# Kernel optimization log

Hardware: AMD Instinct MI355X
Metric: run time of the kernel (lower is better)

Reference implementation:

```python
import jax, jax.numpy as jnp
import numpy as np

B, C, N, K = 4, 64, 8192, 16
OUT = 128

def setup_inputs() -> dict:
    key = jax.random.key(0)
    k1, k2, k3, k4 = jax.random.split(key, 4)
    x = jax.random.normal(k1, (B, C, N, 1), dtype=jnp.float32)
    edge_index = jax.random.randint(k2, (2, B, N, K), 0, N)
    # BasicConv([2C, OUT]) is a 1x1 Conv2d -> weight [OUT, 2C], bias [OUT]
    W_nn = jax.random.normal(k3, (OUT, 2 * C), dtype=jnp.float32) * 0.02
    b_nn = jax.random.normal(k4, (OUT,), dtype=jnp.float32) * 0.02
    return {"x": x, "edge_index": edge_index, "W_nn": W_nn, "b_nn": b_nn}

def _gather_nodes(x2, idx):
    # x2: [B, C, N], idx: [B, N, K] -> [B, C, N, K]
    return jax.vmap(lambda xb, ib: xb[:, ib])(x2, idx)

def reference(x, edge_index, W_nn, b_nn):
    b, c, n, _ = x.shape
    x2 = x[:, :, :, 0]                      # [B, C, N]
    x_i = _gather_nodes(x2, edge_index[1])  # [B, C, N, K]
    x_j = _gather_nodes(x2, edge_index[0])  # [B, C, N, K]
    x_j = jnp.max(x_j - x_i, axis=-1, keepdims=True)  # [B, C, N, 1]
    # interleave channels: cat([x.unsqueeze(2), x_j.unsqueeze(2)], dim=2).reshape(b, 2c, n, 1)
    h = jnp.concatenate([x[:, :, None], x_j[:, :, None]], axis=2).reshape(b, 2 * c, n, 1)
    # BasicConv: 1x1 conv + bias + ReLU
    out = jnp.einsum('oc,bcn->bon', W_nn, h[:, :, :, 0]) + b_nn[None, :, None]
    return jax.nn.relu(out)[:, :, :, None]  # [B, OUT, N, 1]
```

## Files before the change

### kernel.cpp

```cpp
#include <hip/hip_runtime.h>
#include <cstddef>

#define BB 4
#define CC 64
#define NN 8192
#define KK 16
#define OO 128

#define SW 136
#define SH 136

typedef __attribute__((ext_vector_type(8))) short bf16x8;
typedef __attribute__((ext_vector_type(4))) float f32x4;

__device__ __forceinline__ unsigned short f2b(float f) {
    unsigned u = __builtin_bit_cast(unsigned, f);
    unsigned r = (u + 0x7fffu + ((u >> 16) & 1u)) >> 16;
    return (unsigned short)r;
}

__device__ __forceinline__ float bclo(unsigned d) {
    return __builtin_bit_cast(float, d << 16);
}
__device__ __forceinline__ float bchi(unsigned d) {
    return __builtin_bit_cast(float, d & 0xffff0000u);
}

__global__ __launch_bounds__(256) void transpose_kernel(
        const float* __restrict__ x, unsigned short* __restrict__ xt,
        const float* __restrict__ W, unsigned short* __restrict__ Wbf) {
    __shared__ float tile[64][65];
    const int b  = blockIdx.y;
    const int n0 = blockIdx.x * 64;
    const int t  = threadIdx.x;
    const int ln = t & 63;
    const int r  = t >> 6;

    const float* xb = x + (size_t)b * CC * NN;
    #pragma unroll
    for (int s = 0; s < 64; s += 4) {
        int c = s + r;
        tile[c][ln] = xb[(size_t)c * NN + n0 + ln];
    }
    __syncthreads();
    unsigned short* xtb = xt + ((size_t)b * NN + n0) * CC;
    #pragma unroll
    for (int s = 0; s < 64; s += 4) {
        int n = s + r;
        xtb[n * CC + ln] = f2b(tile[ln][n]);
    }

    if (b == 0 && blockIdx.x < 16) {
        int idx = blockIdx.x * 1024 + t * 4;
        float4 v = *reinterpret_cast<const float4*>(W + idx);
        ushort4 o;
        o.x = f2b(v.x); o.y = f2b(v.y); o.z = f2b(v.z); o.w = f2b(v.w);
        *reinterpret_cast<ushort4*>(Wbf + idx) = o;
    }
}

__global__ __launch_bounds__(256) void main_kernel(
        const unsigned short* __restrict__ xt,
        const unsigned short* __restrict__ Wbf,
        const int*            __restrict__ eidx,
        const float*          __restrict__ bias,
        float*                __restrict__ out) {
    __shared__ unsigned short Wl[128 * SW];
    __shared__ unsigned short hl[64 * SH];
    __shared__ int eL[2048];

    const int t    = threadIdx.x;
    const int lane = t & 63;
    const int w    = t >> 6;
    const int b    = blockIdx.y;
    const int n_base = blockIdx.x * 64;

    const int* e0 = eidx + ((size_t)b * NN + n_base) * KK;
    const int* e1 = e0 + (size_t)BB * NN * KK;
    *reinterpret_cast<int4*>(&eL[t * 4])        = *reinterpret_cast<const int4*>(e0 + t * 4);
    *reinterpret_cast<int4*>(&eL[1024 + t * 4]) = *reinterpret_cast<const int4*>(e1 + t * 4);

    #pragma unroll
    for (int it = 0; it < 8; it++) {
        int flat = it * 2048 + t * 8;
        int row = flat >> 7, col = flat & 127;
        *reinterpret_cast<int4*>(&Wl[row * SW + col]) =
            *reinterpret_cast<const int4*>(Wbf + flat);
    }
    __syncthreads();

    const unsigned short* xtb = xt + (size_t)b * NN * CC;
    const int g = lane >> 3;
    const int p = lane & 7;

    #pragma unroll
    for (int bt = 0; bt < 2; bt++) {
        const int nl = w * 16 + bt * 8 + g;
        uint4 xr = *reinterpret_cast<const uint4*>(xtb + (size_t)(n_base + nl) * CC + p * 8);

        float m[8];
        #pragma unroll
        for (int j = 0; j < 8; j++) m[j] = -1e30f;

        #pragma unroll
        for (int k = 0; k < KK; k++) {
            int ij = eL[nl * KK + k];
            int ii = eL[1024 + nl * KK + k];
            uint4 xj = *reinterpret_cast<const uint4*>(xtb + (size_t)ij * CC + p * 8);
            uint4 xi = *reinterpret_cast<const uint4*>(xtb + (size_t)ii * CC + p * 8);
            m[0] = fmaxf(m[0], bclo(xj.x) - bclo(xi.x));
            m[1] = fmaxf(m[1], bchi(xj.x) - bchi(xi.x));
            m[2] = fmaxf(m[2], bclo(xj.y) - bclo(xi.y));
            m[3] = fmaxf(m[3], bchi(xj.y) - bchi(xi.y));
            m[4] = fmaxf(m[4], bclo(xj.z) - bclo(xi.z));
            m[5] = fmaxf(m[5], bchi(xj.z) - bchi(xi.z));
            m[6] = fmaxf(m[6], bclo(xj.w) - bclo(xi.w));
            m[7] = fmaxf(m[7], bchi(xj.w) - bchi(xi.w));
        }

        unsigned xs[8];
        xs[0] = xr.x & 0xffffu; xs[1] = xr.x >> 16;
        xs[2] = xr.y & 0xffffu; xs[3] = xr.y >> 16;
        xs[4] = xr.z & 0xffffu; xs[5] = xr.z >> 16;
        xs[6] = xr.w & 0xffffu; xs[7] = xr.w >> 16;
        unsigned od[8];
        #pragma unroll
        for (int j = 0; j < 8; j++)
            od[j] = xs[j] | ((unsigned)f2b(m[j]) << 16);

        unsigned short* dst = &hl[nl * SH + p * 16];
        uint4 lo, hi;
        lo.x = od[0]; lo.y = od[1]; lo.z = od[2]; lo.w = od[3];
        hi.x = od[4]; hi.y = od[5]; hi.z = od[6]; hi.w = od[7];
        *reinterpret_cast<uint4*>(dst)     = lo;
        *reinterpret_cast<uint4*>(dst + 8) = hi;
    }
    __syncthreads();

    const int quad = lane >> 4;
    const int l15  = lane & 15;
    const int o0w  = w * 32;

    bf16x8 afr[2][4];
    #pragma unroll
    for (int ot = 0; ot < 2; ot++)
        #pragma unroll
        for (int ks = 0; ks < 4; ks++) {
            const unsigned short* ap = &Wl[(o0w + ot * 16 + l15) * SW + ks * 32 + quad * 8];
            afr[ot][ks] = *reinterpret_cast<const bf16x8*>(ap);
        }

    #pragma unroll
    for (int nt = 0; nt < 4; nt++) {
        f32x4 acc0 = {0.f, 0.f, 0.f, 0.f};
        f32x4 acc1 = {0.f, 0.f, 0.f, 0.f};
        #pragma unroll
        for (int ks = 0; ks < 4; ks++) {
            const unsigned short* bp = &hl[(nt * 16 + l15) * SH + ks * 32 + quad * 8];
            bf16x8 bfr = *reinterpret_cast<const bf16x8*>(bp);
            acc0 = __builtin_amdgcn_mfma_f32_16x16x32_bf16(afr[0][ks], bfr, acc0, 0, 0, 0);
            acc1 = __builtin_amdgcn_mfma_f32_16x16x32_bf16(afr[1][ks], bfr, acc1, 0, 0, 0);
        }
        int n_g = n_base + nt * 16 + l15;
        #pragma unroll
        for (int r = 0; r < 4; r++) {
            int o_a = o0w + quad * 4 + r;
            int o_b = o0w + 16 + quad * 4 + r;
            float va = acc0[r] + bias[o_a];
            float vb = acc1[r] + bias[o_b];
            out[((size_t)b * OO + o_a) * NN + n_g] = fmaxf(va, 0.f);
            out[((size_t)b * OO + o_b) * NN + n_g] = fmaxf(vb, 0.f);
        }
    }
}

extern "C" void kernel_launch(void* const* d_in, const int* in_sizes, int n_in,
                              void* d_out, int out_size, void* d_ws, size_t ws_size,
                              hipStream_t stream) {
    const float* x    = (const float*)d_in[0];
    const int*   eidx = (const int*)d_in[1];
    const float* W    = (const float*)d_in[2];
    const float* bias = (const float*)d_in[3];
    float* out = (float*)d_out;

    unsigned short* xt  = (unsigned short*)d_ws;
    unsigned short* Wbf = (unsigned short*)((char*)d_ws + 4 * 1024 * 1024);

    dim3 blk(256);
    dim3 grid(NN / 64, BB);
    transpose_kernel<<<grid, blk, 0, stream>>>(x, xt, W, Wbf);
    main_kernel<<<grid, blk, 0, stream>>>(xt, Wbf, eidx, bias, out);
}
```

Measured before the change: 82.46 us.

## Use 512-thread blocks, drop shared W staging, load MFMA A-fragments from global

The main kernel now runs 512 threads per block, so each thread handles one node's gather-max instead of two and each wave computes 16 output channels instead of 32. The 34 KB shared-memory copy of the weight matrix is removed; each wave loads its A-fragments and bias vector directly from global memory (L2-resident) before the barrier. The aim is to cut shared-memory use and the W staging work, allowing more resident waves to hide gather latency. In exchange, the redundant global W reads and smaller per-wave MFMA tiles add some overhead.

```diff
diff --git a/kernel.cpp b/kernel.cpp
--- a/kernel.cpp
+++ b/kernel.cpp
@@ -7,7 +7,6 @@
 #define KK 16
 #define OO 128
 
-#define SW 136
 #define SH 136
 
 typedef __attribute__((ext_vector_type(8))) short bf16x8;
@@ -59,13 +58,12 @@
     }
 }
 
-__global__ __launch_bounds__(256) void main_kernel(
+__global__ __launch_bounds__(512, 4) void main_kernel(
         const unsigned short* __restrict__ xt,
         const unsigned short* __restrict__ Wbf,
         const int*            __restrict__ eidx,
         const float*          __restrict__ bias,
         float*                __restrict__ out) {
-    __shared__ unsigned short Wl[128 * SW];
     __shared__ unsigned short hl[64 * SH];
     __shared__ int eL[2048];
 
@@ -75,59 +73,66 @@
     const int b    = blockIdx.y;
     const int n_base = blockIdx.x * 64;
 
+    const int quad = lane >> 4;
+    const int l15  = lane & 15;
+    const int o0   = w * 16;
+
+    bf16x8 afr[4];
+    #pragma unroll
+    for (int ks = 0; ks < 4; ks++)
+        afr[ks] = *reinterpret_cast<const bf16x8*>(
+            Wbf + (o0 + l15) * 128 + ks * 32 + quad * 8);
+    f32x4 bv = *reinterpret_cast<const f32x4*>(bias + o0 + quad * 4);
+
     const int* e0 = eidx + ((size_t)b * NN + n_base) * KK;
     const int* e1 = e0 + (size_t)BB * NN * KK;
-    *reinterpret_cast<int4*>(&eL[t * 4])        = *reinterpret_cast<const int4*>(e0 + t * 4);
-    *reinterpret_cast<int4*>(&eL[1024 + t * 4]) = *reinterpret_cast<const int4*>(e1 + t * 4);
+    if (t < 256) {
+        *reinterpret_cast<int4*>(&eL[t * 4]) =
+            *reinterpret_cast<const int4*>(e0 + t * 4);
+    } else {
+        int u = t - 256;
+        *reinterpret_cast<int4*>(&eL[1024 + u * 4]) =
+            *reinterpret_cast<const int4*>(e1 + u * 4);
+    }
+
+    const unsigned short* xtb = xt + (size_t)b * NN * CC;
+    const int nl = t >> 3;
+    const int p  = t & 7;
+    uint4 xr = *reinterpret_cast<const uint4*>(xtb + (size_t)(n_base + nl) * CC + p * 8);
+
+    __syncthreads();
+
+    float m[8];
+    #pragma unroll
+    for (int j = 0; j < 8; j++) m[j] = -1e30f;
 
     #pragma unroll
-    for (int it = 0; it < 8; it++) {
-        int flat = it * 2048 + t * 8;
-        int row = flat >> 7, col = flat & 127;
-        *reinterpret_cast<int4*>(&Wl[row * SW + col]) =
-            *reinterpret_cast<const int4*>(Wbf + flat);
+    for (int k = 0; k < KK; k++) {
+        int ij = eL[nl * KK + k];
+        int ii = eL[1024 + nl * KK + k];
+        uint4 xj = *reinterpret_cast<const uint4*>(xtb + (size_t)ij * CC + p * 8);
+        uint4 xi = *reinterpret_cast<const uint4*>(xtb + (size_t)ii * CC + p * 8);
+        m[0] = fmaxf(m[0], bclo(xj.x) - bclo(xi.x));
+        m[1] = fmaxf(m[1], bchi(xj.x) - bchi(xi.x));
+        m[2] = fmaxf(m[2], bclo(xj.y) - bclo(xi.y));
+        m[3] = fmaxf(m[3], bchi(xj.y) - bchi(xi.y));
+        m[4] = fmaxf(m[4], bclo(xj.z) - bclo(xi.z));
+        m[5] = fmaxf(m[5], bchi(xj.z) - bchi(xi.z));
+        m[6] = fmaxf(m[6], bclo(xj.w) - bclo(xi.w));
+        m[7] = fmaxf(m[7], bchi(xj.w) - bchi(xi.w));
     }
-    __syncthreads();
 
-    const unsigned short* xtb = xt + (size_t)b * NN * CC;
-    const int g = lane >> 3;
-    const int p = lane & 7;
+    unsigned xs[8];
+    xs[0] = xr.x & 0xffffu; xs[1] = xr.x >> 16;
+    xs[2] = xr.y & 0xffffu; xs[3] = xr.y >> 16;
+    xs[4] = xr.z & 0xffffu; xs[5] = xr.z >> 16;
+    xs[6] = xr.w & 0xffffu; xs[7] = xr.w >> 16;
+    unsigned od[8];
+    #pragma unroll
+    for (int j = 0; j < 8; j++)
+        od[j] = xs[j] | ((unsigned)f2b(m[j]) << 16);
 
-    #pragma unroll
-    for (int bt = 0; bt < 2; bt++) {
-        const int nl = w * 16 + bt * 8 + g;
-        uint4 xr = *reinterpret_cast<const uint4*>(xtb + (size_t)(n_base + nl) * CC + p * 8);
-
-        float m[8];
-        #pragma unroll
-        for (int j = 0; j < 8; j++) m[j] = -1e30f;
-
-        #pragma unroll
-        for (int k = 0; k < KK; k++) {
-            int ij = eL[nl * KK + k];
-            int ii = eL[1024 + nl * KK + k];
-            uint4 xj = *reinterpret_cast<const uint4*>(xtb + (size_t)ij * CC + p * 8);
-            uint4 xi = *reinterpret_cast<const uint4*>(xtb + (size_t)ii * CC + p * 8);
-            m[0] = fmaxf(m[0], bclo(xj.x) - bclo(xi.x));
-            m[1] = fmaxf(m[1], bchi(xj.x) - bchi(xi.x));
-            m[2] = fmaxf(m[2], bclo(xj.y) - bclo(xi.y));
-            m[3] = fmaxf(m[3], bchi(xj.y) - bchi(xi.y));
-            m[4] = fmaxf(m[4], bclo(xj.z) - bclo(xi.z));
-            m[5] = fmaxf(m[5], bchi(xj.z) - bchi(xi.z));
-            m[6] = fmaxf(m[6], bclo(xj.w) - bclo(xi.w));
-            m[7] = fmaxf(m[7], bchi(xj.w) - bchi(xi.w));
-        }
-
-        unsigned xs[8];
-        xs[0] = xr.x & 0xffffu; xs[1] = xr.x >> 16;
-        xs[2] = xr.y & 0xffffu; xs[3] = xr.y >> 16;
-        xs[4] = xr.z & 0xffffu; xs[5] = xr.z >> 16;
-        xs[6] = xr.w & 0xffffu; xs[7] = xr.w >> 16;
-        unsigned od[8];
-        #pragma unroll
-        for (int j = 0; j < 8; j++)
-            od[j] = xs[j] | ((unsigned)f2b(m[j]) << 16);
-
+    {
         unsigned short* dst = &hl[nl * SH + p * 16];
         uint4 lo, hi;
         lo.x = od[0]; lo.y = od[1]; lo.z = od[2]; lo.w = od[3];
@@ -137,39 +142,21 @@
     }
     __syncthreads();
 
-    const int quad = lane >> 4;
-    const int l15  = lane & 15;
-    const int o0w  = w * 32;
-
-    bf16x8 afr[2][4];
-    #pragma unroll
-    for (int ot = 0; ot < 2; ot++)
-        #pragma unroll
-        for (int ks = 0; ks < 4; ks++) {
-            const unsigned short* ap = &Wl[(o0w + ot * 16 + l15) * SW + ks * 32 + quad * 8];
-            afr[ot][ks] = *reinterpret_cast<const bf16x8*>(ap);
-        }
-
     #pragma unroll
     for (int nt = 0; nt < 4; nt++) {
-        f32x4 acc0 = {0.f, 0.f, 0.f, 0.f};
-        f32x4 acc1 = {0.f, 0.f, 0.f, 0.f};
+        f32x4 acc = {0.f, 0.f, 0.f, 0.f};
         #pragma unroll
         for (int ks = 0; ks < 4; ks++) {
             const unsigned short* bp = &hl[(nt * 16 + l15) * SH + ks * 32 + quad * 8];
             bf16x8 bfr = *reinterpret_cast<const bf16x8*>(bp);
-            acc0 = __builtin_amdgcn_mfma_f32_16x16x32_bf16(afr[0][ks], bfr, acc0, 0, 0, 0);
-            acc1 = __builtin_amdgcn_mfma_f32_16x16x32_bf16(afr[1][ks], bfr, acc1, 0, 0, 0);
+            acc = __builtin_amdgcn_mfma_f32_16x16x32_bf16(afr[ks], bfr, acc, 0, 0, 0);
         }
         int n_g = n_base + nt * 16 + l15;
         #pragma unroll
         for (int r = 0; r < 4; r++) {
-            int o_a = o0w + quad * 4 + r;
-            int o_b = o0w + 16 + quad * 4 + r;
-            float va = acc0[r] + bias[o_a];
-            float vb = acc1[r] + bias[o_b];
-            out[((size_t)b * OO + o_a) * NN + n_g] = fmaxf(va, 0.f);
-            out[((size_t)b * OO + o_b) * NN + n_g] = fmaxf(vb, 0.f);
+            int o = o0 + quad * 4 + r;
+            float v = acc[r] + bv[r];
+            out[((size_t)b * OO + o) * NN + n_g] = fmaxf(v, 0.f);
         }
     }
 }
@@ -186,8 +173,6 @@
     unsigned short* xt  = (unsigned short*)d_ws;
     unsigned short* Wbf = (unsigned short*)((char*)d_ws + 4 * 1024 * 1024);
 
-    dim3 blk(256);
-    dim3 grid(NN / 64, BB);
-    transpose_kernel<<<grid, blk, 0, stream>>>(x, xt, W, Wbf);
-    main_kernel<<<grid, blk, 0, stream>>>(xt, Wbf, eidx, bias, out);
+    transpose_kernel<<<dim3(NN / 64, BB), dim3(256), 0, stream>>>(x, xt, W, Wbf);
+    main_kernel<<<dim3(NN / 64, BB), dim3(512), 0, stream>>>(xt, Wbf, eidx, bias, out);
 }
```

Result: slower. 85.40 us (+3.6%).
